# Optimization experiments

Hardware: AMD Instinct MI355X
Metric: run time of the kernel (lower is better)

## Reference

```python
import jax, jax.numpy as jnp
import numpy as np

N_NODES = 100000
N_EDGES = 1600000
DIM_IN, DIM_HID, DIM_OUT = 64, 128, 40


def setup_inputs() -> dict:
    key = jax.random.key(0)
    ks = jax.random.split(key, 6)
    x = jax.random.normal(ks[0], (N_NODES, DIM_IN), dtype=jnp.float32)
    edge_index = jax.random.randint(ks[1], (2, N_EDGES), 0, N_NODES, dtype=jnp.int64)
    s_in = 1.0 / np.sqrt(DIM_IN)
    s_hid = 1.0 / np.sqrt(DIM_HID)
    W1l = jax.random.normal(ks[2], (DIM_HID, DIM_IN), dtype=jnp.float32) * s_in
    W1r = jax.random.normal(ks[3], (DIM_HID, DIM_IN), dtype=jnp.float32) * s_in
    b1 = jnp.zeros((DIM_HID,), dtype=jnp.float32)
    W2l = jax.random.normal(ks[4], (DIM_OUT, DIM_HID), dtype=jnp.float32) * s_hid
    W2r = jax.random.normal(ks[5], (DIM_OUT, DIM_HID), dtype=jnp.float32) * s_hid
    b2 = jnp.zeros((DIM_OUT,), dtype=jnp.float32)
    return {"x": x, "edge_index": edge_index, "W1l": W1l, "b1": b1,
            "W1r": W1r, "W2l": W2l, "b2": b2, "W2r": W2r}


def _sage_conv(h, src, dst, Wl, bl, Wr, n_nodes):
    # mean aggregation of source-node features into target nodes
    msg = h[src]                                      # [E, d]
    agg = jax.ops.segment_sum(msg, dst, num_segments=n_nodes)
    cnt = jax.ops.segment_sum(jnp.ones((src.shape[0],), h.dtype), dst,
                              num_segments=n_nodes)
    agg = agg / jnp.maximum(cnt, 1.0)[:, None]        # [N, d]
    # PyG SAGEConv: lin_l(agg) + bias + lin_r(x) (root weight, no bias)
    return agg @ Wl.T + bl + h @ Wr.T


def reference(x, edge_index, W1l, b1, W1r, W2l, b2, W2r):
    src, dst = edge_index[0], edge_index[1]
    n = x.shape[0]
    h = _sage_conv(x, src, dst, W1l, b1, W1r, n)
    h = jax.nn.relu(h)
    out = _sage_conv(h, src, dst, W2l, b2, W2r, n)
    return jax.nn.log_softmax(out, axis=-1)
```

## Files before the change

kernel.cpp:

```cpp
#include <hip/hip_runtime.h>
#include <math.h>

#define NN 100000
#define DI 64
#define DH 128
#define DO 40

#define NBUCK 512
#define NPB 196
#define CAP 3712
#define CAPP 5120
#define EPB 4096
#define TPB_S 512
#define KE (EPB / TPB_S)

typedef __attribute__((ext_vector_type(8))) short bf16x8;
typedef __attribute__((ext_vector_type(4))) float f32x4;
typedef __attribute__((ext_vector_type(2))) float f32x2;

__device__ __forceinline__ unsigned short bf16r(float a) {
    unsigned u = __float_as_uint(a);
    u = (u + 0x7FFF + ((u >> 16) & 1)) >> 16;
    return (unsigned short)u;
}
__device__ __forceinline__ unsigned bf16pair(float a, float b) {
    return (unsigned)bf16r(a) | ((unsigned)bf16r(b) << 16);
}
__device__ __forceinline__ float bflo(unsigned u) { return __uint_as_float(u << 16); }
__device__ __forceinline__ float bfhi(unsigned u) { return __uint_as_float(u & 0xFFFF0000u); }

__global__ __launch_bounds__(TPB_S) void setup_scatter_kernel(
        const float* __restrict__ x, const float* __restrict__ W1l,
        const float* __restrict__ W1r, const float* __restrict__ W2l,
        const float* __restrict__ W2r,
        unsigned* __restrict__ xb, unsigned short* __restrict__ WB1,
        unsigned short* __restrict__ WB2, unsigned* __restrict__ p2,
        const int* __restrict__ src, const int* __restrict__ dst,
        int* __restrict__ bcur, int* __restrict__ eb,
        int nbe, int E, int N) {
    __shared__ int h[NBUCK];
    int t = threadIdx.x;
    if ((int)blockIdx.x < nbe) {
        if (t < NBUCK) h[t] = 0;
        __syncthreads();
        int base = blockIdx.x * EPB;
        int end = base + EPB; if (end > E) end = E;
        int dloc[KE];
#pragma unroll
        for (int k = 0; k < KE; k++) {
            int i = base + t + k * TPB_S;
            dloc[k] = (i < end) ? dst[i] : -1;
        }
#pragma unroll
        for (int k = 0; k < KE; k++)
            if (dloc[k] >= 0) atomicAdd(&h[(unsigned)dloc[k] / NPB], 1);
        __syncthreads();
        if (t < NBUCK) {
            int v = h[t];
            h[t] = v ? (atomicAdd(&bcur[t], v) + t * CAP) : 0;
        }
        __syncthreads();
#pragma unroll
        for (int k = 0; k < KE; k++) {
            int d = dloc[k];
            if (d >= 0) {
                unsigned bk = (unsigned)d / NPB;
                int local = d - (int)bk * NPB;
                int pos = atomicAdd(&h[bk], 1);
                eb[pos] = (local << 17) | src[base + t + k * TPB_S];
            }
        }
    } else {
        int idx = (blockIdx.x - nbe) * TPB_S + t;
        if (idx < (N + 1) * 32) {
            if (idx < N * 32) {
                float2 f = ((const float2*)x)[idx];
                xb[idx] = bf16pair(f.x, f.y);
            } else {
                xb[idx] = 0;
            }
        }
        if (idx < 16384) {
            int j = idx & 7, lane = (idx >> 3) & 63, ks = (idx >> 9) & 3, nt = idx >> 11;
            int k = ks * 32 + (lane >> 4) * 8 + j;
            int n = nt * 16 + (lane & 15);
            float v = (k < DI) ? W1l[n * DI + k] : W1r[n * DI + (k - DI)];
            WB1[idx] = bf16r(v);
        }
        if (idx >= 16384 && idx < 16384 + 10240) {
            int idx2 = idx - 16384;
            int j = idx2 & 7, lane = (idx2 >> 3) & 63, ks = (idx2 >> 9) & 3, nt = idx2 >> 11;
            int k = ks * 32 + (lane >> 4) * 8 + j;
            int n = nt * 16 + (lane & 15);
            float v = (n < DO) ? W2l[n * DH + k] : W2r[(n - DO) * DH + k];
            WB2[idx2] = bf16r(v);
        }
        if (idx < 10) p2[(size_t)N * 10 + idx] = 0;
    }
}

__global__ __launch_bounds__(256) void bucket_fill_kernel(const int* __restrict__ eb,
                                                          const int* __restrict__ bend,
                                                          int* __restrict__ rowptr,
                                                          int* __restrict__ cntg,
                                                          float* __restrict__ inv,
                                                          int* __restrict__ col, int N) {
    __shared__ int scnt[256];
    __shared__ int scur[256];
    __shared__ int sbase[256];
    int b = blockIdx.x, t = threadIdx.x;
    int ebeg = b * CAP, eend = ebeg + bend[b];
    scnt[t] = 0;
    __syncthreads();
    for (int i = ebeg + t; i < eend; i += 256)
        atomicAdd(&scnt[eb[i] >> 17], 1);
    __syncthreads();
    int myc = scnt[t];
    int pc = (myc + 7) & ~7;
    scnt[t] = pc;
    __syncthreads();
    for (int off = 1; off < 256; off <<= 1) {
        int tmp = (t >= off) ? scnt[t - off] : 0;
        __syncthreads();
        scnt[t] += tmp;
        __syncthreads();
    }
    int excl = scnt[t] - pc;
    int base = b * CAPP + excl;
    int node = b * NPB + t;
    if (t < NPB && node < N) {
        rowptr[node] = base;
        cntg[node] = myc;
        inv[node] = 1.0f / (float)(myc > 0 ? myc : 1);
    }
    scur[t] = base;
    sbase[t] = base;
    __syncthreads();
    for (int i = ebeg + t; i < eend; i += 256) {
        int pk = eb[i];
        int pos = atomicAdd(&scur[pk >> 17], 1);
        col[pos] = pk & 0x1FFFF;
    }
    __syncthreads();
    if (t < NPB) {
        int bs = sbase[t];
        for (int i = myc; i < pc; i++) col[bs + i] = NN;
    }
}

__global__ __launch_bounds__(256) void agg_gemm12_kernel(
        const unsigned* __restrict__ xb, const int* __restrict__ rowptr,
        const int* __restrict__ cnt, const float* __restrict__ inv,
        const int* __restrict__ col,
        const unsigned short* __restrict__ WB1, const float* __restrict__ b1,
        const unsigned short* __restrict__ WB2, const float* __restrict__ b2,
        unsigned* __restrict__ p2, float* __restrict__ selfp, int N) {
    __shared__ unsigned short sh[64][136];
    int t = threadIdx.x;
    int w = t >> 6, lane = t & 63;
    int lw = w * 16;
    int g8 = (t >> 3) & 7;
    int chunk = t & 7;
    int rbase = blockIdx.x * 64 + lw;

#pragma unroll
    for (int it = 0; it < 2; ++it) {
        int lr = lw + g8 + it * 8;
        int n = blockIdx.x * 64 + lr;
        float a[8];
#pragma unroll
        for (int j = 0; j < 8; j++) a[j] = 0.f;
        float invn = 0.f;
        uint4 u = make_uint4(0, 0, 0, 0);
        if (n < N) {
            int beg = rowptr[n], deg = cnt[n];
            int degp = (deg + 3) & ~3;
            int4 c = *(const int4*)(col + beg);
            for (int i = 0; i < degp; i += 4) {
                int4 cn = *(const int4*)(col + beg + i + 4);
                uint4 u0 = *(const uint4*)(xb + (size_t)c.x * 32 + chunk * 4);
                uint4 u1 = *(const uint4*)(xb + (size_t)c.y * 32 + chunk * 4);
                uint4 u2 = *(const uint4*)(xb + (size_t)c.z * 32 + chunk * 4);
                uint4 u3 = *(const uint4*)(xb + (size_t)c.w * 32 + chunk * 4);
                a[0] += bflo(u0.x) + bflo(u1.x) + bflo(u2.x) + bflo(u3.x);
                a[1] += bfhi(u0.x) + bfhi(u1.x) + bfhi(u2.x) + bfhi(u3.x);
                a[2] += bflo(u0.y) + bflo(u1.y) + bflo(u2.y) + bflo(u3.y);
                a[3] += bfhi(u0.y) + bfhi(u1.y) + bfhi(u2.y) + bfhi(u3.y);
                a[4] += bflo(u0.z) + bflo(u1.z) + bflo(u2.z) + bflo(u3.z);
                a[5] += bfhi(u0.z) + bfhi(u1.z) + bfhi(u2.z) + bfhi(u3.z);
                a[6] += bflo(u0.w) + bflo(u1.w) + bflo(u2.w) + bflo(u3.w);
                a[7] += bfhi(u0.w) + bfhi(u1.w) + bfhi(u2.w) + bfhi(u3.w);
                c = cn;
            }
            invn = inv[n];
            u = *(const uint4*)(xb + (size_t)n * 32 + chunk * 4);
        }
        uint4 o;
        o.x = bf16pair(a[0] * invn, a[1] * invn);
        o.y = bf16pair(a[2] * invn, a[3] * invn);
        o.z = bf16pair(a[4] * invn, a[5] * invn);
        o.w = bf16pair(a[6] * invn, a[7] * invn);
        *(uint4*)&sh[lr][chunk * 8] = o;
        *(uint4*)&sh[lr][64 + chunk * 8] = u;
    }
    asm volatile("" ::: "memory");

    int quad = lane >> 4, m = lane & 15;
    f32x4 acc[8];
#pragma unroll
    for (int nt = 0; nt < 8; nt++) acc[nt] = (f32x4)(0.f);
#pragma unroll
    for (int ks = 0; ks < 4; ks++) {
        bf16x8 a = *(const bf16x8*)(&sh[lw + m][ks * 32 + quad * 8]);
#pragma unroll
        for (int nt = 0; nt < 8; nt++) {
            bf16x8 b = *(const bf16x8*)(WB1 + ((size_t)(nt * 4 + ks) * 64 + lane) * 8);
            acc[nt] = __builtin_amdgcn_mfma_f32_16x16x32_bf16(a, b, acc[nt], 0, 0, 0);
        }
    }
    asm volatile("" ::: "memory");
#pragma unroll
    for (int nt = 0; nt < 8; nt++) {
        int colj = nt * 16 + m;
        float bj = b1[colj];
#pragma unroll
        for (int r = 0; r < 4; r++) {
            sh[lw + quad * 4 + r][colj] = bf16r(fmaxf(acc[nt][r] + bj, 0.f));
        }
    }
    asm volatile("" ::: "memory");

    f32x4 acc2[5];
#pragma unroll
    for (int nt = 0; nt < 5; nt++) acc2[nt] = (f32x4)(0.f);
#pragma unroll
    for (int ks = 0; ks < 4; ks++) {
        bf16x8 a = *(const bf16x8*)(&sh[lw + m][ks * 32 + quad * 8]);
#pragma unroll
        for (int nt = 0; nt < 5; nt++) {
            bf16x8 b = *(const bf16x8*)(WB2 + ((size_t)(nt * 4 + ks) * 64 + lane) * 8);
            acc2[nt] = __builtin_amdgcn_mfma_f32_16x16x32_bf16(a, b, acc2[nt], 0, 0, 0);
        }
    }
    asm volatile("" ::: "memory");
    float* stw = (float*)&sh[lw][0];
#pragma unroll
    for (int nt = 0; nt < 5; nt++) {
        int colj = nt * 16 + m;
#pragma unroll
        for (int r = 0; r < 4; r++) {
            int row = rbase + quad * 4 + r;
            float v = acc2[nt][r];
            if (colj < 40) {
                stw[(quad * 4 + r) * 41 + colj] = v;
            } else if (row < N) {
                selfp[(size_t)row * 40 + (colj - 40)] = v + b2[colj - 40];
            }
        }
    }
    asm volatile("" ::: "memory");
    for (int i = lane; i < 160; i += 64) {
        int lr = i / 10, dw = i - lr * 10;
        int grow = rbase + lr;
        if (grow < N) {
            float v0 = stw[lr * 41 + dw * 4 + 0], v1 = stw[lr * 41 + dw * 4 + 1];
            float v2 = stw[lr * 41 + dw * 4 + 2], v3 = stw[lr * 41 + dw * 4 + 3];
            unsigned u = __builtin_amdgcn_cvt_pk_fp8_f32(v0, v1, 0u, false);
            u = __builtin_amdgcn_cvt_pk_fp8_f32(v2, v3, u, true);
            p2[(size_t)grow * 10 + dw] = u;
        }
    }
}

__global__ void agg2_softmax_kernel(const unsigned* __restrict__ p2,
                                    const float* __restrict__ selfp,
                                    const int* __restrict__ rowptr,
                                    const int* __restrict__ cnt,
                                    const float* __restrict__ inv,
                                    const int* __restrict__ col,
                                    float* __restrict__ out, int N) {
    int n = (blockIdx.x * 256 + threadIdx.x) >> 3;
    int chunk = threadIdx.x & 7;
    if (n >= N) return;
    int beg = rowptr[n], deg = cnt[n];
    int degp = (deg + 7) & ~7;
    bool vc = (chunk < 5);
    float a[8];
#pragma unroll
    for (int j = 0; j < 8; j++) a[j] = 0.f;
    int4 c0 = *(const int4*)(col + beg);
    int4 c1 = *(const int4*)(col + beg + 4);
    for (int i = 0; i < degp; i += 8) {
        int4 n0 = *(const int4*)(col + beg + i + 8);
        int4 n1 = *(const int4*)(col + beg + i + 12);
        int ss[8] = {c0.x, c0.y, c0.z, c0.w, c1.x, c1.y, c1.z, c1.w};
        if (vc) {
            uint2 uu[8];
#pragma unroll
            for (int k = 0; k < 8; k++)
                uu[k] = *(const uint2*)(p2 + (size_t)ss[k] * 10 + chunk * 2);
#pragma unroll
            for (int k = 0; k < 8; k++) {
                f32x2 d;
                d = __builtin_amdgcn_cvt_pk_f32_fp8(uu[k].x, false); a[0] += d.x; a[1] += d.y;
                d = __builtin_amdgcn_cvt_pk_f32_fp8(uu[k].x, true);  a[2] += d.x; a[3] += d.y;
                d = __builtin_amdgcn_cvt_pk_f32_fp8(uu[k].y, false); a[4] += d.x; a[5] += d.y;
                d = __builtin_amdgcn_cvt_pk_f32_fp8(uu[k].y, true);  a[6] += d.x; a[7] += d.y;
            }
        }
        c0 = n0; c1 = n1;
    }
    float invn = inv[n];
    float v[8];
    if (vc) {
        float4 s0 = *(const float4*)(selfp + (size_t)n * DO + chunk * 8);
        float4 s1 = *(const float4*)(selfp + (size_t)n * DO + chunk * 8 + 4);
        v[0] = a[0] * invn + s0.x; v[1] = a[1] * invn + s0.y;
        v[2] = a[2] * invn + s0.z; v[3] = a[3] * invn + s0.w;
        v[4] = a[4] * invn + s1.x; v[5] = a[5] * invn + s1.y;
        v[6] = a[6] * invn + s1.z; v[7] = a[7] * invn + s1.w;
    } else {
#pragma unroll
        for (int j = 0; j < 8; j++) v[j] = 0.f;
    }
    float mv = -INFINITY;
    if (vc) {
#pragma unroll
        for (int j = 0; j < 8; j++) mv = fmaxf(mv, v[j]);
    }
#pragma unroll
    for (int off = 1; off <= 4; off <<= 1) mv = fmaxf(mv, __shfl_xor(mv, off, 8));
    float es = 0.f;
    if (vc) {
#pragma unroll
        for (int j = 0; j < 8; j++) es += expf(v[j] - mv);
    }
#pragma unroll
    for (int off = 1; off <= 4; off <<= 1) es += __shfl_xor(es, off, 8);
    if (vc) {
        float ls = mv + logf(es);
        float4 o0, o1;
        o0.x = v[0] - ls; o0.y = v[1] - ls; o0.z = v[2] - ls; o0.w = v[3] - ls;
        o1.x = v[4] - ls; o1.y = v[5] - ls; o1.z = v[6] - ls; o1.w = v[7] - ls;
        *(float4*)(out + (size_t)n * DO + chunk * 8) = o0;
        *(float4*)(out + (size_t)n * DO + chunk * 8 + 4) = o1;
    }
}

extern "C" void kernel_launch(void* const* d_in, const int* in_sizes, int n_in,
                              void* d_out, int out_size, void* d_ws, size_t ws_size,
                              hipStream_t stream) {
    const float* x   = (const float*)d_in[0];
    const int*  ei   = (const int*)d_in[1];
    const float* W1l = (const float*)d_in[2];
    const float* b1  = (const float*)d_in[3];
    const float* W1r = (const float*)d_in[4];
    const float* W2l = (const float*)d_in[5];
    const float* b2  = (const float*)d_in[6];
    const float* W2r = (const float*)d_in[7];
    float* out = (float*)d_out;

    const int E = in_sizes[1] / 2;
    const int N = NN;
    const int* src = ei;
    const int* dst = ei + E;
    const int nbe = (E + EPB - 1) / EPB;
    const int nsetup = ((N + 1) * 32 + TPB_S - 1) / TPB_S;

    size_t off = 0;
    auto alloc = [&](size_t nf) { size_t o = off; off += (nf + 63) & ~(size_t)63; return o; };
    size_t o_bcur   = alloc(NBUCK);
    size_t o_eb     = alloc((size_t)NBUCK * CAP);
    size_t o_col    = alloc((size_t)NBUCK * CAPP + 64);
    size_t o_rowptr = alloc(N);
    size_t o_cnt    = alloc(N);
    size_t o_inv    = alloc(N);
    size_t o_xb     = alloc((size_t)(N + 1) * 32);
    size_t o_p2     = alloc((size_t)(N + 1) * 10);
    size_t o_selfp  = alloc((size_t)N * DO);
    size_t o_wb1    = alloc(16384 / 2);
    size_t o_wb2    = alloc(10240 / 2);
    (void)ws_size;

    float* ws = (float*)d_ws;
    int* bcur   = (int*)(ws + o_bcur);
    int* eb     = (int*)(ws + o_eb);
    int* col    = (int*)(ws + o_col);
    int* rowptr = (int*)(ws + o_rowptr);
    int* cnt    = (int*)(ws + o_cnt);
    float* inv  = ws + o_inv;
    unsigned* xb = (unsigned*)(ws + o_xb);
    unsigned* p2 = (unsigned*)(ws + o_p2);
    float* selfp = ws + o_selfp;
    unsigned short* WB1 = (unsigned short*)(ws + o_wb1);
    unsigned short* WB2 = (unsigned short*)(ws + o_wb2);

    hipMemsetAsync(bcur, 0, NBUCK * sizeof(int), stream);

    setup_scatter_kernel<<<nbe + nsetup, TPB_S, 0, stream>>>(
        x, W1l, W1r, W2l, W2r, xb, WB1, WB2, p2, src, dst, bcur, eb, nbe, E, N);

    bucket_fill_kernel<<<NBUCK, 256, 0, stream>>>(eb, bcur, rowptr, cnt, inv, col, N);

    agg_gemm12_kernel<<<(N + 63) / 64, 256, 0, stream>>>(
        xb, rowptr, cnt, inv, col, WB1, b1, WB2, b2, p2, selfp, N);

    agg2_softmax_kernel<<<(N * 8 + 255) / 256, 256, 0, stream>>>(p2, selfp, rowptr, cnt, inv, col, out, N);
}
```

Before: 196.4 us.

## Sort nodes by degree for layer-1 aggregation to balance wavefront work

```diff
diff --git a/kernel.cpp b/kernel.cpp
--- a/kernel.cpp
+++ b/kernel.cpp
@@ -104,7 +104,8 @@
                                                           int* __restrict__ rowptr,
                                                           int* __restrict__ cntg,
                                                           float* __restrict__ inv,
-                                                          int* __restrict__ col, int N) {
+                                                          int* __restrict__ col,
+                                                          int* __restrict__ ghist, int N) {
     __shared__ int scnt[256];
     __shared__ int scur[256];
     __shared__ int sbase[256];
@@ -132,6 +133,8 @@
         rowptr[node] = base;
         cntg[node] = myc;
         inv[node] = 1.0f / (float)(myc > 0 ? myc : 1);
+        int key = 255 - (myc > 255 ? 255 : myc);
+        atomicAdd(&ghist[key], 1);
     }
     scur[t] = base;
     sbase[t] = base;
@@ -148,10 +151,38 @@
     }
 }
 
+__global__ __launch_bounds__(256) void prefix_kernel(const int* __restrict__ ghist,
+                                                     int* __restrict__ gbase) {
+    __shared__ int s[256];
+    int t = threadIdx.x;
+    int v0 = ghist[t];
+    s[t] = v0;
+    __syncthreads();
+    for (int off = 1; off < 256; off <<= 1) {
+        int v = (t >= off) ? s[t - off] : 0;
+        __syncthreads();
+        s[t] += v;
+        __syncthreads();
+    }
+    gbase[t] = s[t] - v0;
+}
+
+__global__ __launch_bounds__(256) void perm_kernel(const int* __restrict__ cnt,
+                                                   int* __restrict__ gbase,
+                                                   int* __restrict__ perm, int N) {
+    int i = blockIdx.x * 256 + threadIdx.x;
+    if (i < N) {
+        int d = cnt[i];
+        int key = 255 - (d > 255 ? 255 : d);
+        int pos = atomicAdd(&gbase[key], 1);
+        perm[pos] = i;
+    }
+}
+
 __global__ __launch_bounds__(256) void agg_gemm12_kernel(
         const unsigned* __restrict__ xb, const int* __restrict__ rowptr,
         const int* __restrict__ cnt, const float* __restrict__ inv,
-        const int* __restrict__ col,
+        const int* __restrict__ col, const int* __restrict__ perm,
         const unsigned short* __restrict__ WB1, const float* __restrict__ b1,
         const unsigned short* __restrict__ WB2, const float* __restrict__ b2,
         unsigned* __restrict__ p2, float* __restrict__ selfp, int N) {
@@ -161,23 +192,22 @@
     int lw = w * 16;
     int g8 = (t >> 3) & 7;
     int chunk = t & 7;
-    int rbase = blockIdx.x * 64 + lw;
 
 #pragma unroll
     for (int it = 0; it < 2; ++it) {
         int lr = lw + g8 + it * 8;
-        int n = blockIdx.x * 64 + lr;
+        int pos = blockIdx.x * 64 + lr;
+        bool valid = (pos < N);
+        int n = valid ? perm[pos] : NN;
         float a[8];
 #pragma unroll
         for (int j = 0; j < 8; j++) a[j] = 0.f;
         float invn = 0.f;
-        uint4 u = make_uint4(0, 0, 0, 0);
-        if (n < N) {
+        if (valid) {
             int beg = rowptr[n], deg = cnt[n];
             int degp = (deg + 3) & ~3;
-            int4 c = *(const int4*)(col + beg);
             for (int i = 0; i < degp; i += 4) {
-                int4 cn = *(const int4*)(col + beg + i + 4);
+                int4 c = *(const int4*)(col + beg + i);
                 uint4 u0 = *(const uint4*)(xb + (size_t)c.x * 32 + chunk * 4);
                 uint4 u1 = *(const uint4*)(xb + (size_t)c.y * 32 + chunk * 4);
                 uint4 u2 = *(const uint4*)(xb + (size_t)c.z * 32 + chunk * 4);
@@ -190,11 +220,10 @@
                 a[5] += bfhi(u0.z) + bfhi(u1.z) + bfhi(u2.z) + bfhi(u3.z);
                 a[6] += bflo(u0.w) + bflo(u1.w) + bflo(u2.w) + bflo(u3.w);
                 a[7] += bfhi(u0.w) + bfhi(u1.w) + bfhi(u2.w) + bfhi(u3.w);
-                c = cn;
             }
             invn = inv[n];
-            u = *(const uint4*)(xb + (size_t)n * 32 + chunk * 4);
-        }
+        }
+        uint4 u = *(const uint4*)(xb + (size_t)n * 32 + chunk * 4);
         uint4 o;
         o.x = bf16pair(a[0] * invn, a[1] * invn);
         o.y = bf16pair(a[2] * invn, a[3] * invn);
@@ -249,11 +278,12 @@
         int colj = nt * 16 + m;
 #pragma unroll
         for (int r = 0; r < 4; r++) {
-            int row = rbase + quad * 4 + r;
+            int pos = blockIdx.x * 64 + lw + quad * 4 + r;
             float v = acc2[nt][r];
             if (colj < 40) {
                 stw[(quad * 4 + r) * 41 + colj] = v;
-            } else if (row < N) {
+            } else if (pos < N) {
+                int row = perm[pos];
                 selfp[(size_t)row * 40 + (colj - 40)] = v + b2[colj - 40];
             }
         }
@@ -261,8 +291,9 @@
     asm volatile("" ::: "memory");
     for (int i = lane; i < 160; i += 64) {
         int lr = i / 10, dw = i - lr * 10;
-        int grow = rbase + lr;
-        if (grow < N) {
+        int pos = blockIdx.x * 64 + lw + lr;
+        if (pos < N) {
+            int grow = perm[pos];
             float v0 = stw[lr * 41 + dw * 4 + 0], v1 = stw[lr * 41 + dw * 4 + 1];
             float v2 = stw[lr * 41 + dw * 4 + 2], v3 = stw[lr * 41 + dw * 4 + 3];
             unsigned u = __builtin_amdgcn_cvt_pk_fp8_f32(v0, v1, 0u, false);
@@ -288,12 +319,10 @@
     float a[8];
 #pragma unroll
     for (int j = 0; j < 8; j++) a[j] = 0.f;
-    int4 c0 = *(const int4*)(col + beg);
-    int4 c1 = *(const int4*)(col + beg + 4);
     for (int i = 0; i < degp; i += 8) {
-        int4 n0 = *(const int4*)(col + beg + i + 8);
-        int4 n1 = *(const int4*)(col + beg + i + 12);
-        int ss[8] = {c0.x, c0.y, c0.z, c0.w, c1.x, c1.y, c1.z, c1.w};
+        int ss[8];
+#pragma unroll
+        for (int k = 0; k < 8; k++) ss[k] = col[beg + i + k];
         if (vc) {
             uint2 uu[8];
 #pragma unroll
@@ -308,7 +337,6 @@
                 d = __builtin_amdgcn_cvt_pk_f32_fp8(uu[k].y, true);  a[6] += d.x; a[7] += d.y;
             }
         }
-        c0 = n0; c1 = n1;
     }
     float invn = inv[n];
     float v[8];
@@ -370,6 +398,9 @@
     size_t off = 0;
     auto alloc = [&](size_t nf) { size_t o = off; off += (nf + 63) & ~(size_t)63; return o; };
     size_t o_bcur   = alloc(NBUCK);
+    size_t o_ghist  = alloc(256);
+    size_t o_gbase  = alloc(256);
+    size_t o_perm   = alloc(100032);
     size_t o_eb     = alloc((size_t)NBUCK * CAP);
     size_t o_col    = alloc((size_t)NBUCK * CAPP + 64);
     size_t o_rowptr = alloc(N);
@@ -384,6 +415,9 @@
 
     float* ws = (float*)d_ws;
     int* bcur   = (int*)(ws + o_bcur);
+    int* ghist  = (int*)(ws + o_ghist);
+    int* gbase  = (int*)(ws + o_gbase);
+    int* perm   = (int*)(ws + o_perm);
     int* eb     = (int*)(ws + o_eb);
     int* col    = (int*)(ws + o_col);
     int* rowptr = (int*)(ws + o_rowptr);
@@ -395,15 +429,18 @@
     unsigned short* WB1 = (unsigned short*)(ws + o_wb1);
     unsigned short* WB2 = (unsigned short*)(ws + o_wb2);
 
-    hipMemsetAsync(bcur, 0, NBUCK * sizeof(int), stream);
+    hipMemsetAsync(bcur, 0, (NBUCK + 256) * sizeof(int), stream);
 
     setup_scatter_kernel<<<nbe + nsetup, TPB_S, 0, stream>>>(
         x, W1l, W1r, W2l, W2r, xb, WB1, WB2, p2, src, dst, bcur, eb, nbe, E, N);
 
-    bucket_fill_kernel<<<NBUCK, 256, 0, stream>>>(eb, bcur, rowptr, cnt, inv, col, N);
+    bucket_fill_kernel<<<NBUCK, 256, 0, stream>>>(eb, bcur, rowptr, cnt, inv, col, ghist, N);
+
+    prefix_kernel<<<1, 256, 0, stream>>>(ghist, gbase);
+    perm_kernel<<<(N + 255) / 256, 256, 0, stream>>>(cnt, gbase, perm, N);
 
     agg_gemm12_kernel<<<(N + 63) / 64, 256, 0, stream>>>(
-        xb, rowptr, cnt, inv, col, WB1, b1, WB2, b2, p2, selfp, N);
+        xb, rowptr, cnt, inv, col, perm, WB1, b1, WB2, b2, p2, selfp, N);
 
     agg2_softmax_kernel<<<(N * 8 + 255) / 256, 256, 0, stream>>>(p2, selfp, rowptr, cnt, inv, col, out, N);
 }
```

Result: slower. 723.1 us (+268.2%).

## Replace bucketed edge sort with global-atomic count, scan and scatter CSR build

Applied to the files above, without the earlier changes.

```diff
diff --git a/kernel.cpp b/kernel.cpp
--- a/kernel.cpp
+++ b/kernel.cpp
@@ -8,7 +8,6 @@
 
 #define NBUCK 512
 #define NPB 196
-#define CAP 3712
 #define CAPP 5120
 #define EPB 4096
 #define TPB_S 512
@@ -29,20 +28,16 @@
 __device__ __forceinline__ float bflo(unsigned u) { return __uint_as_float(u << 16); }
 __device__ __forceinline__ float bfhi(unsigned u) { return __uint_as_float(u & 0xFFFF0000u); }
 
-__global__ __launch_bounds__(TPB_S) void setup_scatter_kernel(
+__global__ __launch_bounds__(TPB_S) void setup_count_kernel(
         const float* __restrict__ x, const float* __restrict__ W1l,
         const float* __restrict__ W1r, const float* __restrict__ W2l,
         const float* __restrict__ W2r,
         unsigned* __restrict__ xb, unsigned short* __restrict__ WB1,
         unsigned short* __restrict__ WB2, unsigned* __restrict__ p2,
-        const int* __restrict__ src, const int* __restrict__ dst,
-        int* __restrict__ bcur, int* __restrict__ eb,
+        const int* __restrict__ dst, int* __restrict__ cnt,
         int nbe, int E, int N) {
-    __shared__ int h[NBUCK];
     int t = threadIdx.x;
     if ((int)blockIdx.x < nbe) {
-        if (t < NBUCK) h[t] = 0;
-        __syncthreads();
         int base = blockIdx.x * EPB;
         int end = base + EPB; if (end > E) end = E;
         int dloc[KE];
@@ -53,23 +48,7 @@
         }
 #pragma unroll
         for (int k = 0; k < KE; k++)
-            if (dloc[k] >= 0) atomicAdd(&h[(unsigned)dloc[k] / NPB], 1);
-        __syncthreads();
-        if (t < NBUCK) {
-            int v = h[t];
-            h[t] = v ? (atomicAdd(&bcur[t], v) + t * CAP) : 0;
-        }
-        __syncthreads();
-#pragma unroll
-        for (int k = 0; k < KE; k++) {
-            int d = dloc[k];
-            if (d >= 0) {
-                unsigned bk = (unsigned)d / NPB;
-                int local = d - (int)bk * NPB;
-                int pos = atomicAdd(&h[bk], 1);
-                eb[pos] = (local << 17) | src[base + t + k * TPB_S];
-            }
-        }
+            if (dloc[k] >= 0) atomicAdd(&cnt[dloc[k]], 1);
     } else {
         int idx = (blockIdx.x - nbe) * TPB_S + t;
         if (idx < (N + 1) * 32) {
@@ -99,52 +78,55 @@
     }
 }
 
-__global__ __launch_bounds__(256) void bucket_fill_kernel(const int* __restrict__ eb,
-                                                          const int* __restrict__ bend,
-                                                          int* __restrict__ rowptr,
-                                                          int* __restrict__ cntg,
-                                                          float* __restrict__ inv,
-                                                          int* __restrict__ col, int N) {
-    __shared__ int scnt[256];
-    __shared__ int scur[256];
-    __shared__ int sbase[256];
+__global__ __launch_bounds__(256) void rowptr_kernel(const int* __restrict__ cnt,
+                                                     int* __restrict__ rowptr,
+                                                     int* __restrict__ cur,
+                                                     float* __restrict__ inv,
+                                                     int* __restrict__ col, int N) {
+    __shared__ int s[256];
     int b = blockIdx.x, t = threadIdx.x;
-    int ebeg = b * CAP, eend = ebeg + bend[b];
-    scnt[t] = 0;
-    __syncthreads();
-    for (int i = ebeg + t; i < eend; i += 256)
-        atomicAdd(&scnt[eb[i] >> 17], 1);
-    __syncthreads();
-    int myc = scnt[t];
-    int pc = (myc + 7) & ~7;
-    scnt[t] = pc;
+    int node = b * NPB + t;
+    bool valid = (t < NPB && node < N);
+    int c = valid ? cnt[node] : 0;
+    int pc = (c + 7) & ~7;
+    s[t] = pc;
     __syncthreads();
     for (int off = 1; off < 256; off <<= 1) {
-        int tmp = (t >= off) ? scnt[t - off] : 0;
+        int v = (t >= off) ? s[t - off] : 0;
         __syncthreads();
-        scnt[t] += tmp;
+        s[t] += v;
         __syncthreads();
     }
-    int excl = scnt[t] - pc;
+    int excl = s[t] - pc;
     int base = b * CAPP + excl;
-    int node = b * NPB + t;
-    if (t < NPB && node < N) {
+    if (valid) {
         rowptr[node] = base;
-        cntg[node] = myc;
-        inv[node] = 1.0f / (float)(myc > 0 ? myc : 1);
-    }
-    scur[t] = base;
-    sbase[t] = base;
-    __syncthreads();
-    for (int i = ebeg + t; i < eend; i += 256) {
-        int pk = eb[i];
-        int pos = atomicAdd(&scur[pk >> 17], 1);
-        col[pos] = pk & 0x1FFFF;
-    }
-    __syncthreads();
-    if (t < NPB) {
-        int bs = sbase[t];
-        for (int i = myc; i < pc; i++) col[bs + i] = NN;
+        cur[node] = base;
+        inv[node] = 1.0f / (float)(c > 0 ? c : 1);
+        for (int i = c; i < pc; i++) col[base + i] = NN;
+    }
+}
+
+__global__ __launch_bounds__(TPB_S) void scatter_kernel(const int* __restrict__ src,
+                                                        const int* __restrict__ dst,
+                                                        int* __restrict__ cur,
+                                                        int* __restrict__ col, int E) {
+    int t = threadIdx.x;
+    int base = blockIdx.x * EPB;
+    int end = base + EPB; if (end > E) end = E;
+    int dloc[KE], sloc[KE];
+#pragma unroll
+    for (int k = 0; k < KE; k++) {
+        int i = base + t + k * TPB_S;
+        dloc[k] = (i < end) ? dst[i] : -1;
+        sloc[k] = (i < end) ? src[i] : 0;
+    }
+#pragma unroll
+    for (int k = 0; k < KE; k++) {
+        if (dloc[k] >= 0) {
+            int pos = atomicAdd(&cur[dloc[k]], 1);
+            col[pos] = sloc[k];
+        }
     }
 }
 
@@ -167,17 +149,17 @@
     for (int it = 0; it < 2; ++it) {
         int lr = lw + g8 + it * 8;
         int n = blockIdx.x * 64 + lr;
+        bool valid = (n < N);
+        int ne = valid ? n : NN;
         float a[8];
 #pragma unroll
         for (int j = 0; j < 8; j++) a[j] = 0.f;
         float invn = 0.f;
-        uint4 u = make_uint4(0, 0, 0, 0);
-        if (n < N) {
+        if (valid) {
             int beg = rowptr[n], deg = cnt[n];
             int degp = (deg + 3) & ~3;
-            int4 c = *(const int4*)(col + beg);
             for (int i = 0; i < degp; i += 4) {
-                int4 cn = *(const int4*)(col + beg + i + 4);
+                int4 c = *(const int4*)(col + beg + i);
                 uint4 u0 = *(const uint4*)(xb + (size_t)c.x * 32 + chunk * 4);
                 uint4 u1 = *(const uint4*)(xb + (size_t)c.y * 32 + chunk * 4);
                 uint4 u2 = *(const uint4*)(xb + (size_t)c.z * 32 + chunk * 4);
@@ -190,11 +172,10 @@
                 a[5] += bfhi(u0.z) + bfhi(u1.z) + bfhi(u2.z) + bfhi(u3.z);
                 a[6] += bflo(u0.w) + bflo(u1.w) + bflo(u2.w) + bflo(u3.w);
                 a[7] += bfhi(u0.w) + bfhi(u1.w) + bfhi(u2.w) + bfhi(u3.w);
-                c = cn;
             }
             invn = inv[n];
-            u = *(const uint4*)(xb + (size_t)n * 32 + chunk * 4);
-        }
+        }
+        uint4 u = *(const uint4*)(xb + (size_t)ne * 32 + chunk * 4);
         uint4 o;
         o.x = bf16pair(a[0] * invn, a[1] * invn);
         o.y = bf16pair(a[2] * invn, a[3] * invn);
@@ -288,12 +269,10 @@
     float a[8];
 #pragma unroll
     for (int j = 0; j < 8; j++) a[j] = 0.f;
-    int4 c0 = *(const int4*)(col + beg);
-    int4 c1 = *(const int4*)(col + beg + 4);
     for (int i = 0; i < degp; i += 8) {
-        int4 n0 = *(const int4*)(col + beg + i + 8);
-        int4 n1 = *(const int4*)(col + beg + i + 12);
-        int ss[8] = {c0.x, c0.y, c0.z, c0.w, c1.x, c1.y, c1.z, c1.w};
+        int ss[8];
+#pragma unroll
+        for (int k = 0; k < 8; k++) ss[k] = col[beg + i + k];
         if (vc) {
             uint2 uu[8];
 #pragma unroll
@@ -308,7 +287,6 @@
                 d = __builtin_amdgcn_cvt_pk_f32_fp8(uu[k].y, true);  a[6] += d.x; a[7] += d.y;
             }
         }
-        c0 = n0; c1 = n1;
     }
     float invn = inv[n];
     float v[8];
@@ -369,12 +347,11 @@
 
     size_t off = 0;
     auto alloc = [&](size_t nf) { size_t o = off; off += (nf + 63) & ~(size_t)63; return o; };
-    size_t o_bcur   = alloc(NBUCK);
-    size_t o_eb     = alloc((size_t)NBUCK * CAP);
+    size_t o_cnt    = alloc(N);
+    size_t o_cur    = alloc(N);
+    size_t o_rowptr = alloc(N);
+    size_t o_inv    = alloc(N);
     size_t o_col    = alloc((size_t)NBUCK * CAPP + 64);
-    size_t o_rowptr = alloc(N);
-    size_t o_cnt    = alloc(N);
-    size_t o_inv    = alloc(N);
     size_t o_xb     = alloc((size_t)(N + 1) * 32);
     size_t o_p2     = alloc((size_t)(N + 1) * 10);
     size_t o_selfp  = alloc((size_t)N * DO);
@@ -383,24 +360,25 @@
     (void)ws_size;
 
     float* ws = (float*)d_ws;
-    int* bcur   = (int*)(ws + o_bcur);
-    int* eb     = (int*)(ws + o_eb);
+    int* cnt    = (int*)(ws + o_cnt);
+    int* cur    = (int*)(ws + o_cur);
+    int* rowptr = (int*)(ws + o_rowptr);
+    float* inv  = ws + o_inv;
     int* col    = (int*)(ws + o_col);
-    int* rowptr = (int*)(ws + o_rowptr);
-    int* cnt    = (int*)(ws + o_cnt);
-    float* inv  = ws + o_inv;
     unsigned* xb = (unsigned*)(ws + o_xb);
     unsigned* p2 = (unsigned*)(ws + o_p2);
     float* selfp = ws + o_selfp;
     unsigned short* WB1 = (unsigned short*)(ws + o_wb1);
     unsigned short* WB2 = (unsigned short*)(ws + o_wb2);
 
-    hipMemsetAsync(bcur, 0, NBUCK * sizeof(int), stream);
-
-    setup_scatter_kernel<<<nbe + nsetup, TPB_S, 0, stream>>>(
-        x, W1l, W1r, W2l, W2r, xb, WB1, WB2, p2, src, dst, bcur, eb, nbe, E, N);
-
-    bucket_fill_kernel<<<NBUCK, 256, 0, stream>>>(eb, bcur, rowptr, cnt, inv, col, N);
+    hipMemsetAsync(cnt, 0, N * sizeof(int), stream);
+
+    setup_count_kernel<<<nbe + nsetup, TPB_S, 0, stream>>>(
+        x, W1l, W1r, W2l, W2r, xb, WB1, WB2, p2, dst, cnt, nbe, E, N);
+
+    rowptr_kernel<<<NBUCK, 256, 0, stream>>>(cnt, rowptr, cur, inv, col, N);
+
+    scatter_kernel<<<nbe, TPB_S, 0, stream>>>(src, dst, cur, col, E);
 
     agg_gemm12_kernel<<<(N + 63) / 64, 256, 0, stream>>>(
         xb, rowptr, cnt, inv, col, WB1, b1, WB2, b2, p2, selfp, N);
```

Result: slower. 352.7 us (+79.6%).

## Count node degrees with global atomics during scatter and widen bucket fill

Applied to the files above, without the earlier changes.

```diff
diff --git a/kernel.cpp b/kernel.cpp
--- a/kernel.cpp
+++ b/kernel.cpp
@@ -36,7 +36,7 @@
         unsigned* __restrict__ xb, unsigned short* __restrict__ WB1,
         unsigned short* __restrict__ WB2, unsigned* __restrict__ p2,
         const int* __restrict__ src, const int* __restrict__ dst,
-        int* __restrict__ bcur, int* __restrict__ eb,
+        int* __restrict__ bcur, int* __restrict__ eb, int* __restrict__ cnt,
         int nbe, int E, int N) {
     __shared__ int h[NBUCK];
     int t = threadIdx.x;
@@ -52,8 +52,12 @@
             dloc[k] = (i < end) ? dst[i] : -1;
         }
 #pragma unroll
-        for (int k = 0; k < KE; k++)
-            if (dloc[k] >= 0) atomicAdd(&h[(unsigned)dloc[k] / NPB], 1);
+        for (int k = 0; k < KE; k++) {
+            if (dloc[k] >= 0) {
+                atomicAdd(&h[(unsigned)dloc[k] / NPB], 1);
+                atomicAdd(&cnt[dloc[k]], 1);
+            }
+        }
         __syncthreads();
         if (t < NBUCK) {
             int v = h[t];
@@ -99,52 +103,45 @@
     }
 }
 
-__global__ __launch_bounds__(256) void bucket_fill_kernel(const int* __restrict__ eb,
+__global__ __launch_bounds__(512) void bucket_fill_kernel(const int* __restrict__ eb,
                                                           const int* __restrict__ bend,
+                                                          const int* __restrict__ cnt,
                                                           int* __restrict__ rowptr,
-                                                          int* __restrict__ cntg,
                                                           float* __restrict__ inv,
                                                           int* __restrict__ col, int N) {
-    __shared__ int scnt[256];
+    __shared__ int s[256];
     __shared__ int scur[256];
-    __shared__ int sbase[256];
     int b = blockIdx.x, t = threadIdx.x;
     int ebeg = b * CAP, eend = ebeg + bend[b];
-    scnt[t] = 0;
-    __syncthreads();
-    for (int i = ebeg + t; i < eend; i += 256)
-        atomicAdd(&scnt[eb[i] >> 17], 1);
-    __syncthreads();
-    int myc = scnt[t];
-    int pc = (myc + 7) & ~7;
-    scnt[t] = pc;
+    int node = b * NPB + t;
+    bool valid = (t < NPB && node < N);
+    int c = valid ? cnt[node] : 0;
+    int pc = (c + 7) & ~7;
+    if (t < 256) s[t] = pc;
     __syncthreads();
     for (int off = 1; off < 256; off <<= 1) {
-        int tmp = (t >= off) ? scnt[t - off] : 0;
+        int v = (t < 256 && t >= off) ? s[t - off] : 0;
         __syncthreads();
-        scnt[t] += tmp;
+        if (t < 256) s[t] += v;
         __syncthreads();
     }
-    int excl = scnt[t] - pc;
-    int base = b * CAPP + excl;
-    int node = b * NPB + t;
-    if (t < NPB && node < N) {
-        rowptr[node] = base;
-        cntg[node] = myc;
-        inv[node] = 1.0f / (float)(myc > 0 ? myc : 1);
-    }
-    scur[t] = base;
-    sbase[t] = base;
+    int base = 0;
+    if (t < 256) {
+        base = b * CAPP + s[t] - pc;
+        scur[t] = base;
+        if (valid) {
+            rowptr[node] = base;
+            inv[node] = 1.0f / (float)(c > 0 ? c : 1);
+        }
+    }
     __syncthreads();
-    for (int i = ebeg + t; i < eend; i += 256) {
+    for (int i = ebeg + t; i < eend; i += 512) {
         int pk = eb[i];
         int pos = atomicAdd(&scur[pk >> 17], 1);
         col[pos] = pk & 0x1FFFF;
     }
-    __syncthreads();
-    if (t < NPB) {
-        int bs = sbase[t];
-        for (int i = myc; i < pc; i++) col[bs + i] = NN;
+    if (valid) {
+        for (int i = c; i < pc; i++) col[base + i] = NN;
     }
 }
 
@@ -167,17 +164,17 @@
     for (int it = 0; it < 2; ++it) {
         int lr = lw + g8 + it * 8;
         int n = blockIdx.x * 64 + lr;
+        bool valid = (n < N);
+        int ne = valid ? n : NN;
         float a[8];
 #pragma unroll
         for (int j = 0; j < 8; j++) a[j] = 0.f;
         float invn = 0.f;
-        uint4 u = make_uint4(0, 0, 0, 0);
-        if (n < N) {
+        if (valid) {
             int beg = rowptr[n], deg = cnt[n];
             int degp = (deg + 3) & ~3;
-            int4 c = *(const int4*)(col + beg);
             for (int i = 0; i < degp; i += 4) {
-                int4 cn = *(const int4*)(col + beg + i + 4);
+                int4 c = *(const int4*)(col + beg + i);
                 uint4 u0 = *(const uint4*)(xb + (size_t)c.x * 32 + chunk * 4);
                 uint4 u1 = *(const uint4*)(xb + (size_t)c.y * 32 + chunk * 4);
                 uint4 u2 = *(const uint4*)(xb + (size_t)c.z * 32 + chunk * 4);
@@ -190,11 +187,10 @@
                 a[5] += bfhi(u0.z) + bfhi(u1.z) + bfhi(u2.z) + bfhi(u3.z);
                 a[6] += bflo(u0.w) + bflo(u1.w) + bflo(u2.w) + bflo(u3.w);
                 a[7] += bfhi(u0.w) + bfhi(u1.w) + bfhi(u2.w) + bfhi(u3.w);
-                c = cn;
             }
             invn = inv[n];
-            u = *(const uint4*)(xb + (size_t)n * 32 + chunk * 4);
-        }
+        }
+        uint4 u = *(const uint4*)(xb + (size_t)ne * 32 + chunk * 4);
         uint4 o;
         o.x = bf16pair(a[0] * invn, a[1] * invn);
         o.y = bf16pair(a[2] * invn, a[3] * invn);
@@ -288,12 +284,10 @@
     float a[8];
 #pragma unroll
     for (int j = 0; j < 8; j++) a[j] = 0.f;
-    int4 c0 = *(const int4*)(col + beg);
-    int4 c1 = *(const int4*)(col + beg + 4);
     for (int i = 0; i < degp; i += 8) {
-        int4 n0 = *(const int4*)(col + beg + i + 8);
-        int4 n1 = *(const int4*)(col + beg + i + 12);
-        int ss[8] = {c0.x, c0.y, c0.z, c0.w, c1.x, c1.y, c1.z, c1.w};
+        int ss[8];
+#pragma unroll
+        for (int k = 0; k < 8; k++) ss[k] = col[beg + i + k];
         if (vc) {
             uint2 uu[8];
 #pragma unroll
@@ -308,7 +302,6 @@
                 d = __builtin_amdgcn_cvt_pk_f32_fp8(uu[k].y, true);  a[6] += d.x; a[7] += d.y;
             }
         }
-        c0 = n0; c1 = n1;
     }
     float invn = inv[n];
     float v[8];
@@ -370,10 +363,10 @@
     size_t off = 0;
     auto alloc = [&](size_t nf) { size_t o = off; off += (nf + 63) & ~(size_t)63; return o; };
     size_t o_bcur   = alloc(NBUCK);
+    size_t o_cnt    = alloc(N);
     size_t o_eb     = alloc((size_t)NBUCK * CAP);
     size_t o_col    = alloc((size_t)NBUCK * CAPP + 64);
     size_t o_rowptr = alloc(N);
-    size_t o_cnt    = alloc(N);
     size_t o_inv    = alloc(N);
     size_t o_xb     = alloc((size_t)(N + 1) * 32);
     size_t o_p2     = alloc((size_t)(N + 1) * 10);
@@ -384,10 +377,10 @@
 
     float* ws = (float*)d_ws;
     int* bcur   = (int*)(ws + o_bcur);
+    int* cnt    = (int*)(ws + o_cnt);
     int* eb     = (int*)(ws + o_eb);
     int* col    = (int*)(ws + o_col);
     int* rowptr = (int*)(ws + o_rowptr);
-    int* cnt    = (int*)(ws + o_cnt);
     float* inv  = ws + o_inv;
     unsigned* xb = (unsigned*)(ws + o_xb);
     unsigned* p2 = (unsigned*)(ws + o_p2);
@@ -395,12 +388,12 @@
     unsigned short* WB1 = (unsigned short*)(ws + o_wb1);
     unsigned short* WB2 = (unsigned short*)(ws + o_wb2);
 
-    hipMemsetAsync(bcur, 0, NBUCK * sizeof(int), stream);
+    hipMemsetAsync(bcur, 0, (NBUCK + N) * sizeof(int), stream);
 
     setup_scatter_kernel<<<nbe + nsetup, TPB_S, 0, stream>>>(
-        x, W1l, W1r, W2l, W2r, xb, WB1, WB2, p2, src, dst, bcur, eb, nbe, E, N);
-
-    bucket_fill_kernel<<<NBUCK, 256, 0, stream>>>(eb, bcur, rowptr, cnt, inv, col, N);
+        x, W1l, W1r, W2l, W2r, xb, WB1, WB2, p2, src, dst, bcur, eb, cnt, nbe, E, N);
+
+    bucket_fill_kernel<<<NBUCK, 512, 0, stream>>>(eb, bcur, cnt, rowptr, inv, col, N);
 
     agg_gemm12_kernel<<<(N + 63) / 64, 256, 0, stream>>>(
         xb, rowptr, cnt, inv, col, WB1, b1, WB2, b2, p2, selfp, N);
```

New measurement: 247.2 us. 1.26x slower.
